# Optimization experiments

Measured on AMD Instinct MI355X. Metric: run time of the kernel, lower is better.

## Reference

```python
import jax, jax.numpy as jnp
import numpy as np

HEADS = 32
K_TOP = 512  # top-k tokens gathered from KV


def conv3d(x, w, b=None, pad=0, groups=1):
    # x: [B,C,D,H,W], w: [O, I/groups, kd,kh,kw]
    out = jax.lax.conv_general_dilated(
        x, w, window_strides=(1, 1, 1), padding=[(pad, pad)] * 3,
        dimension_numbers=("NCDHW", "OIDHW", "NCDHW"), feature_group_count=groups)
    if b is not None:
        out = out + b[None, :, None, None, None]
    return out


def setup_inputs() -> dict:
    key = jax.random.key(0)
    ks = jax.random.split(key, 10)
    B, C, D, H, W = 2, 256, 16, 16, 16
    p = lambda i, shape: (jax.random.normal(ks[i], shape, jnp.float32) * 0.02)
    return {
        "x_kv": jax.random.normal(ks[0], (B, C, D, H, W), jnp.float32),
        "x_q": jax.random.normal(ks[1], (B, C, D, H, W), jnp.float32),
        "w_spa": p(2, (1, 2, 7, 7, 7)),            # SpatialAttention conv, no bias
        "w_kv": p(3, (C, 2 * C)), "b_kv": jnp.zeros((2 * C,), jnp.float32),
        "w_q": p(4, (C, C)), "b_q": jnp.zeros((C,), jnp.float32),
        "w_proj": p(5, (C, C)), "b_proj": jnp.zeros((C,), jnp.float32),
        "w_dw": p(6, (C, 1, 3, 3, 3)), "b_dw": jnp.zeros((C,), jnp.float32),  # depthwise 3x3x3
        "w_pw": p(7, (C, C, 1, 1, 1)), "b_pw": jnp.zeros((C,), jnp.float32),  # pointwise 1x1x1
    }


def reference(x_kv, x_q, w_spa, w_kv, b_kv, w_q, b_q, w_proj, b_proj,
              w_dw, b_dw, w_pw, b_pw):
    B, C, D, H, W = x_kv.shape
    N = D * H * W
    hd = C // HEADS
    scale = hd ** -0.5

    # SpatialAttention: channel mean/max -> conv(2->1, k=7, pad=3) -> sigmoid
    avg = jnp.mean(x_kv, axis=1, keepdims=True)
    mx = jnp.max(x_kv, axis=1, keepdims=True)
    spa = jax.nn.sigmoid(conv3d(jnp.concatenate([avg, mx], axis=1), w_spa, None, pad=3))
    scores = spa.reshape(B, N)                      # [B, N]
    _, idx = jax.lax.top_k(scores, K_TOP)           # [B, K] (descending, like torch.topk)

    # Full K/V projection over all N tokens (as in original), then gather top-k
    xkv_t = x_kv.reshape(B, C, N).transpose(0, 2, 1)        # [B, N, C]
    kv = xkv_t @ w_kv + b_kv                                 # [B, N, 2C]
    k_full, v_full = kv[..., :C], kv[..., C:]
    k_g = jnp.take_along_axis(k_full, idx[:, :, None], axis=1)  # [B, K, C]
    v_g = jnp.take_along_axis(v_full, idx[:, :, None], axis=1)
    k_g = k_g.reshape(B, K_TOP, HEADS, hd).transpose(0, 2, 1, 3)  # [B, h, K, d]
    v_g = v_g.reshape(B, K_TOP, HEADS, hd).transpose(0, 2, 1, 3)

    # Queries over all Nq tokens
    xq_t = x_q.reshape(B, C, N).transpose(0, 2, 1)           # [B, N, C]
    q = (xq_t @ w_q + b_q).reshape(B, N, HEADS, hd).transpose(0, 2, 1, 3)  # [B, h, N, d]

    attn = jax.nn.softmax(jnp.einsum('bhnd,bhkd->bhnk', q, k_g) * scale, axis=-1)
    out = jnp.einsum('bhnk,bhkd->bhnd', attn, v_g)           # [B, h, N, d]
    out = out.transpose(0, 2, 1, 3).reshape(B, N, C)
    out = out @ w_proj + b_proj
    out = out.transpose(0, 2, 1).reshape(B, C, D, H, W)

    # DWconv residual on full (ungathered) V
    v_vol = v_full.transpose(0, 2, 1).reshape(B, C, D, H, W)
    res = conv3d(conv3d(v_vol, w_dw, b_dw, pad=1, groups=C), w_pw, b_pw)
    return out + res
```

## Files before the change

### kernel.cpp

```cpp
#include <hip/hip_runtime.h>
#include <hip/hip_bf16.h>

typedef short bf16x8 __attribute__((ext_vector_type(8)));
typedef float f32x4 __attribute__((ext_vector_type(4)));

constexpr int CN = 256, NV = 4096, KTOP = 512;

static __device__ __forceinline__ unsigned short f2bf(float f) {
  __hip_bfloat16 h = __float2bfloat16(f);
  return *(unsigned short*)&h;
}
static __device__ __forceinline__ unsigned pack2(float a, float b) {
  return (unsigned)f2bf(a) | ((unsigned)f2bf(b) << 16);
}
static __device__ __forceinline__ float bf2f(unsigned short u) {
  return __uint_as_float(((unsigned)u) << 16);
}
static __device__ __forceinline__ unsigned packtrunc(float a, float b) {
  return (__float_as_uint(a) >> 16) | (__float_as_uint(b) & 0xFFFF0000u);
}

__global__ void __launch_bounds__(256) k_tcast2(const float* __restrict__ srcA,
                                                const float* __restrict__ srcB,
                                                unsigned short* __restrict__ dstA,
                                                unsigned short* __restrict__ dstB) {
  __shared__ float tile[64 * 65];
  int z = blockIdx.z, b = z & 1;
  const float* s = (z < 2 ? srcA : srcB) + (size_t)b * CN * NV;
  unsigned short* d = (z < 2 ? dstA : dstB) + (size_t)b * NV * 256;
  int c0 = blockIdx.y * 64, n0 = blockIdx.x * 64;
  int t = threadIdx.x;
  for (int i = 0; i < 16; ++i) {
    int id = i * 256 + t, c = id >> 6, n = id & 63;
    tile[c * 65 + n] = s[(size_t)(c0 + c) * NV + n0 + n];
  }
  __syncthreads();
  int n = t & 63, part = t >> 6;
  unsigned w[8];
#pragma unroll
  for (int k = 0; k < 8; ++k)
    w[k] = pack2(tile[(part * 16 + 2 * k) * 65 + n], tile[(part * 16 + 2 * k + 1) * 65 + n]);
  uint4* p = (uint4*)&d[(size_t)(n0 + n) * 256 + c0 + part * 16];
  p[0] = make_uint4(w[0], w[1], w[2], w[3]);
  p[1] = make_uint4(w[4], w[5], w[6], w[7]);
}

__global__ void __launch_bounds__(256) k_wprep(const float* __restrict__ wkv,
                                               const float* __restrict__ wq,
                                               const float* __restrict__ wproj,
                                               const float* __restrict__ wpw,
                                               unsigned short* __restrict__ wv_t,
                                               unsigned short* __restrict__ wq_t,
                                               unsigned short* __restrict__ wcat,
                                               unsigned short* __restrict__ wk_t) {
  __shared__ float tile[64 * 65];
  int role = blockIdx.z;
  int j0 = blockIdx.x * 64, c0 = blockIdx.y * 64;
  int t = threadIdx.x;
  if (role == 3) {
    int j = t >> 2, part = t & 3;
    const float* s = &wpw[(size_t)(j0 + j) * 256 + c0 + part * 16];
    unsigned w[8];
#pragma unroll
    for (int k = 0; k < 8; ++k) w[k] = pack2(s[2 * k], s[2 * k + 1]);
    uint4* p = (uint4*)&wcat[(size_t)(j0 + j) * 512 + 256 + c0 + part * 16];
    p[0] = make_uint4(w[0], w[1], w[2], w[3]);
    p[1] = make_uint4(w[4], w[5], w[6], w[7]);
    return;
  }
  const float* src; int srcLD, srcOff; unsigned short* dst; int dstLD;
  if (role == 0)      { src = wkv;   srcLD = 512; srcOff = 256; dst = wv_t; dstLD = 256; }
  else if (role == 1) { src = wq;    srcLD = 256; srcOff = 0;   dst = wq_t; dstLD = 256; }
  else if (role == 4) { src = wkv;   srcLD = 512; srcOff = 0;   dst = wk_t; dstLD = 256; }
  else                { src = wproj; srcLD = 256; srcOff = 0;   dst = wcat; dstLD = 512; }
  for (int i = 0; i < 16; ++i) {
    int id = i * 256 + t, c = id >> 6, j = id & 63;
    tile[c * 65 + j] = src[(size_t)(c0 + c) * srcLD + srcOff + j0 + j];
  }
  __syncthreads();
  int j = t & 63, part = t >> 6;
  unsigned w[8];
#pragma unroll
  for (int k = 0; k < 8; ++k)
    w[k] = pack2(tile[(part * 16 + 2 * k) * 65 + j], tile[(part * 16 + 2 * k + 1) * 65 + j]);
  uint4* p = (uint4*)&dst[(size_t)(j0 + j) * dstLD + c0 + part * 16];
  p[0] = make_uint4(w[0], w[1], w[2], w[3]);
  p[1] = make_uint4(w[4], w[5], w[6], w[7]);
}

__global__ void __launch_bounds__(256) k_reduce(const float* __restrict__ xkv,
                                                float* __restrict__ avgmx) {
  __shared__ float ssum[256], smax[256];
  int blk = blockIdx.x;
  int b = blk >> 7, n0 = (blk & 127) * 32;
  int t = threadIdx.x, cg = t >> 5, nl = t & 31;
  int n = n0 + nl;
  const float* p = xkv + (size_t)b * CN * NV + (size_t)cg * 32 * NV + n;
  float s = 0.f, m = -1e30f;
  for (int i = 0; i < 32; ++i) {
    float v = p[(size_t)i * NV];
    s += v; m = fmaxf(m, v);
  }
  ssum[t] = s; smax[t] = m;
  __syncthreads();
  if (cg == 0) {
    for (int g = 1; g < 8; ++g) { s += ssum[g * 32 + nl]; m = fmaxf(m, smax[g * 32 + nl]); }
    avgmx[(b * 2 + 0) * NV + n] = s * (1.0f / 256.0f);
    avgmx[(b * 2 + 1) * NV + n] = m;
  }
}

__global__ void __launch_bounds__(256) k_spa(const float* __restrict__ avgmx,
                                             const float* __restrict__ wspa,
                                             float* __restrict__ scores) {
  __shared__ float vol[2 * 4096];
  __shared__ float ws[686];
  int b = blockIdx.x >> 5, chunk = blockIdx.x & 31;
  int tid = threadIdx.x;
  for (int t = tid; t < 8192; t += 256) vol[t] = avgmx[b * 8192 + t];
  for (int t = tid; t < 686; t += 256) ws[t] = wspa[t];
  __syncthreads();
  int ci = tid & 1;
  int n = chunk * 128 + (tid >> 1);
  int d = n >> 8, h = (n >> 4) & 15, w = n & 15;
  const float* vb = vol + ci * 4096;
  const float* wb = ws + ci * 343;
  float acc = 0.f;
  for (int kd = 0; kd < 7; ++kd) {
    int zd = d - 3 + kd; if ((unsigned)zd >= 16u) continue;
    for (int kh = 0; kh < 7; ++kh) {
      int zh = h - 3 + kh; if ((unsigned)zh >= 16u) continue;
      const float* row = vb + zd * 256 + zh * 16;
      const float* wr = wb + kd * 49 + kh * 7;
#pragma unroll
      for (int kw = 0; kw < 7; ++kw) {
        int zw = w - 3 + kw;
        if ((unsigned)zw < 16u) acc += row[zw] * wr[kw];
      }
    }
  }
  acc += __shfl_xor(acc, 1);
  if (ci == 0) scores[b * NV + n] = 1.0f / (1.0f + expf(-acc));
}

__global__ void __launch_bounds__(1024) k_topk(const float* __restrict__ scores,
                                               int* __restrict__ idx) {
  __shared__ unsigned sv[4096];
  __shared__ int sB;
  __shared__ unsigned sSub, scnt;
  __shared__ unsigned hist[256];
  __shared__ int wsum[16];
  int b = blockIdx.x, tid = threadIdx.x;
  for (int t = tid; t < 4096; t += 1024) sv[t] = __float_as_uint(scores[b * NV + t]);
  if (tid == 0) scnt = 0;
  unsigned prefix = 0;
  int r = 512;
  for (int shift = 24; shift >= 0; shift -= 8) {
    if (tid < 256) hist[tid] = 0;
    __syncthreads();
    unsigned maskhi = (shift == 24) ? 0u : (0xFFFFFFFFu << (shift + 8));
    for (int i = 0; i < 4; ++i) {
      unsigned v = sv[tid + i * 1024];
      if ((v & maskhi) == prefix) atomicAdd(&hist[(v >> shift) & 255], 1u);
    }
    __syncthreads();
    if (tid < 64) {
      int lane = tid;
      unsigned h0 = hist[lane * 4 + 0], h1 = hist[lane * 4 + 1];
      unsigned h2 = hist[lane * 4 + 2], h3 = hist[lane * 4 + 3];
      unsigned s = h0 + h1 + h2 + h3;
      for (int off = 1; off < 64; off <<= 1) {
        unsigned y = __shfl_down(s, off);
        if (lane + off < 64) s += y;
      }
      unsigned tail = __shfl_down(s, 1);
      if (lane == 63) tail = 0;
      unsigned s3 = tail + h3, s2 = s3 + h2, s1 = s2 + h1, s0 = s1 + h0;
      unsigned sx[5] = {s0, s1, s2, s3, tail};
#pragma unroll
      for (int i = 0; i < 4; ++i)
        if (sx[i] >= (unsigned)r && sx[i + 1] < (unsigned)r) { sB = lane * 4 + i; sSub = sx[i + 1]; }
    }
    __syncthreads();
    prefix |= ((unsigned)sB) << shift;
    r -= (int)sSub;
    __syncthreads();
  }
  unsigned vstar = prefix;
  for (int i = 0; i < 4; ++i) {
    int t = tid * 4 + i;
    if (sv[t] > vstar) { unsigned p = atomicAdd(&scnt, 1u); idx[b * KTOP + p] = t; }
  }
  __syncthreads();
  int base = (int)scnt;
  int loc = 0;
  for (int i = 0; i < 4; ++i) loc += (sv[tid * 4 + i] == vstar);
  int lane = tid & 63, w = tid >> 6;
  int x = loc;
  for (int off = 1; off < 64; off <<= 1) {
    int y = __shfl_up(x, off);
    if (lane >= off) x += y;
  }
  if (lane == 63) wsum[w] = x;
  __syncthreads();
  int wbase = 0;
  for (int i = 0; i < w; ++i) wbase += wsum[i];
  int excl = wbase + x - loc;
  for (int i = 0; i < 4; ++i) {
    int t = tid * 4 + i;
    if (sv[t] == vstar) {
      if (excl < r) idx[b * KTOP + base + excl] = t;
      ++excl;
    }
  }
}

__global__ void __launch_bounds__(256) k_qv(const unsigned short* __restrict__ xkv_t,
                                            const unsigned short* __restrict__ xq_t,
                                            const unsigned short* __restrict__ wv_t,
                                            const unsigned short* __restrict__ wq_t,
                                            const float* __restrict__ bkv,
                                            const float* __restrict__ bq,
                                            unsigned short* __restrict__ v_nc,
                                            unsigned short* __restrict__ qh) {
  __shared__ unsigned short Als[128 * 40];
  __shared__ unsigned short Bls[128 * 40];
  int role = blockIdx.z;
  int b = role & 1;
  bool isQ = role >= 2;
  const unsigned short* A = isQ ? wq_t : wv_t;
  const unsigned short* B = (isQ ? xq_t : xkv_t) + (size_t)b * NV * 256;
  const float* bias = isQ ? bq : (bkv + 256);
  int n0 = blockIdx.x * 128, j0 = blockIdx.y * 128;
  int t = threadIdx.x;
  int wave = t >> 6, lane = t & 63;
  int l15 = lane & 15, q = lane >> 4, q8 = q * 8;
  int wj = (wave >> 1) * 64, wn = (wave & 1) * 64;
  f32x4 acc[4][4] = {};
  int ar = t >> 1, ah = t & 1;
  for (int c0 = 0; c0 < 256; c0 += 32) {
    __syncthreads();
    {
      const unsigned short* sa = &A[(size_t)(j0 + ar) * 256 + c0 + ah * 16];
      *(uint4*)&Als[ar * 40 + ah * 16]     = *(const uint4*)&sa[0];
      *(uint4*)&Als[ar * 40 + ah * 16 + 8] = *(const uint4*)&sa[8];
      const unsigned short* sb = &B[(size_t)(n0 + ar) * 256 + c0 + ah * 16];
      *(uint4*)&Bls[ar * 40 + ah * 16]     = *(const uint4*)&sb[0];
      *(uint4*)&Bls[ar * 40 + ah * 16 + 8] = *(const uint4*)&sb[8];
    }
    __syncthreads();
    bf16x8 af[4], bf[4];
#pragma unroll
    for (int mt = 0; mt < 4; ++mt)
      af[mt] = *(const bf16x8*)&Als[(wj + mt * 16 + l15) * 40 + q8];
#pragma unroll
    for (int nt = 0; nt < 4; ++nt)
      bf[nt] = *(const bf16x8*)&Bls[(wn + nt * 16 + l15) * 40 + q8];
#pragma unroll
    for (int mt = 0; mt < 4; ++mt)
#pragma unroll
      for (int nt = 0; nt < 4; ++nt)
        acc[mt][nt] = __builtin_amdgcn_mfma_f32_16x16x32_bf16(af[mt], bf[nt], acc[mt][nt], 0, 0, 0);
  }
#pragma unroll
  for (int mt = 0; mt < 4; ++mt) {
    int jb = j0 + wj + mt * 16 + q * 4;
    float4 b4 = *(const float4*)&bias[jb];
#pragma unroll
    for (int nt = 0; nt < 4; ++nt) {
      int n = n0 + wn + nt * 16 + l15;
      float v0 = acc[mt][nt][0] + b4.x;
      float v1 = acc[mt][nt][1] + b4.y;
      float v2 = acc[mt][nt][2] + b4.z;
      float v3 = acc[mt][nt][3] + b4.w;
      uint2 pk = make_uint2(pack2(v0, v1), pack2(v2, v3));
      if (isQ) {
        int h = jb >> 3, d0 = jb & 7;
        *(uint2*)&qh[((size_t)(b * 32 + h) * NV + n) * 8 + d0] = pk;
      } else {
        *(uint2*)&v_nc[((size_t)b * NV + n) * 256 + jb] = pk;
      }
    }
  }
}

__global__ void __launch_bounds__(256) k_kg(const unsigned short* __restrict__ xkv_t,
                                            const unsigned short* __restrict__ wk_t,
                                            const float* __restrict__ bkv,
                                            const int* __restrict__ map,
                                            unsigned short* __restrict__ kg) {
  __shared__ unsigned short Als[128 * 40];
  __shared__ unsigned short Bls[128 * 40];
  const float kscale = 0.35355339059327373f * 1.4426950408889634f;
  int b = blockIdx.z;
  int m0 = blockIdx.x * 128, j0 = blockIdx.y * 128;
  int t = threadIdx.x;
  int wave = t >> 6, lane = t & 63;
  int l15 = lane & 15, q = lane >> 4, q8 = q * 8;
  int wj = (wave >> 1) * 64, wn = (wave & 1) * 64;
  int ar = t >> 1, ah = t & 1;
  int nrow = map[b * KTOP + m0 + ar];
  const unsigned short* Bbase = xkv_t + (size_t)b * NV * 256;
  f32x4 acc[4][4] = {};
  for (int c0 = 0; c0 < 256; c0 += 32) {
    __syncthreads();
    {
      const unsigned short* sa = &wk_t[(size_t)(j0 + ar) * 256 + c0 + ah * 16];
      *(uint4*)&Als[ar * 40 + ah * 16]     = *(const uint4*)&sa[0];
      *(uint4*)&Als[ar * 40 + ah * 16 + 8] = *(const uint4*)&sa[8];
      const unsigned short* sb = &Bbase[(size_t)nrow * 256 + c0 + ah * 16];
      *(uint4*)&Bls[ar * 40 + ah * 16]     = *(const uint4*)&sb[0];
      *(uint4*)&Bls[ar * 40 + ah * 16 + 8] = *(const uint4*)&sb[8];
    }
    __syncthreads();
    bf16x8 af[4], bfr[4];
#pragma unroll
    for (int mt = 0; mt < 4; ++mt)
      af[mt] = *(const bf16x8*)&Als[(wj + mt * 16 + l15) * 40 + q8];
#pragma unroll
    for (int nt = 0; nt < 4; ++nt)
      bfr[nt] = *(const bf16x8*)&Bls[(wn + nt * 16 + l15) * 40 + q8];
#pragma unroll
    for (int mt = 0; mt < 4; ++mt)
#pragma unroll
      for (int nt = 0; nt < 4; ++nt)
        acc[mt][nt] = __builtin_amdgcn_mfma_f32_16x16x32_bf16(af[mt], bfr[nt], acc[mt][nt], 0, 0, 0);
  }
#pragma unroll
  for (int mt = 0; mt < 4; ++mt) {
    int jb = j0 + wj + mt * 16 + q * 4;
    int h = jb >> 3, d0 = jb & 7;
    float4 b4 = *(const float4*)&bkv[jb];
#pragma unroll
    for (int nt = 0; nt < 4; ++nt) {
      int m = m0 + wn + nt * 16 + l15;
      float v0 = (acc[mt][nt][0] + b4.x) * kscale;
      float v1 = (acc[mt][nt][1] + b4.y) * kscale;
      float v2 = (acc[mt][nt][2] + b4.z) * kscale;
      float v3 = (acc[mt][nt][3] + b4.w) * kscale;
      uint2 pk = make_uint2(pack2(v0, v1), pack2(v2, v3));
      *(uint2*)&kg[((size_t)(b * 32 + h) * KTOP + m) * 8 + d0] = pk;
    }
  }
}

__global__ void __launch_bounds__(256) k_vt(const unsigned short* __restrict__ v_nc,
                                            const int* __restrict__ idx,
                                            unsigned short* __restrict__ vt) {
  int bh = blockIdx.x;
  int b = bh >> 5, h = bh & 31;
  int t = threadIdx.x;
  unsigned short* dst = vt + (size_t)bh * 16 * 512;
  for (int i = t; i < 512; i += 256) dst[8 * 512 + i] = 0x3F80;
  for (int i = t; i < 512 * 7; i += 256) dst[9 * 512 + i] = 0;
  const int* ib = idx + b * KTOP;
  for (int kk = t; kk < 512; kk += 256) {
    uint4 v = *(const uint4*)&v_nc[((size_t)b * NV + ib[kk]) * 256 + h * 8];
    unsigned short tmp[8];
    *(uint4*)tmp = v;
    int kc = kk >> 5, ka = kk & 31;
    int s = (ka < 16) ? ((ka >> 2) * 8 + (ka & 3))
                      : (((ka - 16) >> 2) * 8 + (ka & 3) + 4);
    int col = kc * 32 + s;
#pragma unroll
    for (int d = 0; d < 8; ++d) dst[d * 512 + col] = tmp[d];
  }
}

__global__ void __launch_bounds__(256) k_fattn(const unsigned short* __restrict__ qh,
                                               const unsigned short* __restrict__ kg,
                                               const unsigned short* __restrict__ vt,
                                               unsigned short* __restrict__ aoydw) {
  int bh = blockIdx.x;
  int b = bh >> 5, h = bh & 31;
  int t = threadIdx.x, wave = t >> 6, lane = t & 63;
  int l15 = lane & 15, quad = lane >> 4;
  int n0 = blockIdx.y * 128 + wave * 32;
  bf16x8 q0 = {}, q1 = {};
  if (quad == 0) {
    q0 = *(const bf16x8*)&qh[((size_t)bh * NV + n0 + l15) * 8];
    q1 = *(const bf16x8*)&qh[((size_t)bh * NV + n0 + 16 + l15) * 8];
  }
  const unsigned short* kbase = kg + (size_t)bh * KTOP * 8;
  const unsigned short* vbase = vt + (size_t)bh * 16 * 512;
  f32x4 acc0 = {0.f, 0.f, 0.f, 0.f}, acc1 = {0.f, 0.f, 0.f, 0.f};
  bf16x8 kA0 = {}, kA1 = {};
  if (quad == 0) {
    kA0 = *(const bf16x8*)&kbase[(size_t)l15 * 8];
    kA1 = *(const bf16x8*)&kbase[(size_t)(16 + l15) * 8];
  }
  for (int kc = 0; kc < 16; ++kc) {
    bf16x8 nA0 = {}, nA1 = {};
    if (quad == 0 && kc < 15) {
      nA0 = *(const bf16x8*)&kbase[(size_t)(kc * 32 + 32 + l15) * 8];
      nA1 = *(const bf16x8*)&kbase[(size_t)(kc * 32 + 48 + l15) * 8];
    }
    bf16x8 bV = *(const bf16x8*)&vbase[(size_t)l15 * 512 + kc * 32 + quad * 8];
    f32x4 z = {0.f, 0.f, 0.f, 0.f};
    f32x4 s00 = __builtin_amdgcn_mfma_f32_16x16x32_bf16(kA0, q0, z, 0, 0, 0);
    f32x4 s01 = __builtin_amdgcn_mfma_f32_16x16x32_bf16(kA1, q0, z, 0, 0, 0);
    f32x4 s10 = __builtin_amdgcn_mfma_f32_16x16x32_bf16(kA0, q1, z, 0, 0, 0);
    f32x4 s11 = __builtin_amdgcn_mfma_f32_16x16x32_bf16(kA1, q1, z, 0, 0, 0);
    uint4 P0, P1;
    P0.x = packtrunc(__builtin_amdgcn_exp2f(s00[0]), __builtin_amdgcn_exp2f(s00[1]));
    P0.y = packtrunc(__builtin_amdgcn_exp2f(s00[2]), __builtin_amdgcn_exp2f(s00[3]));
    P0.z = packtrunc(__builtin_amdgcn_exp2f(s01[0]), __builtin_amdgcn_exp2f(s01[1]));
    P0.w = packtrunc(__builtin_amdgcn_exp2f(s01[2]), __builtin_amdgcn_exp2f(s01[3]));
    P1.x = packtrunc(__builtin_amdgcn_exp2f(s10[0]), __builtin_amdgcn_exp2f(s10[1]));
    P1.y = packtrunc(__builtin_amdgcn_exp2f(s10[2]), __builtin_amdgcn_exp2f(s10[3]));
    P1.z = packtrunc(__builtin_amdgcn_exp2f(s11[0]), __builtin_amdgcn_exp2f(s11[1]));
    P1.w = packtrunc(__builtin_amdgcn_exp2f(s11[2]), __builtin_amdgcn_exp2f(s11[3]));
    acc0 = __builtin_amdgcn_mfma_f32_16x16x32_bf16(*(bf16x8*)&P0, bV, acc0, 0, 0, 0);
    acc1 = __builtin_amdgcn_mfma_f32_16x16x32_bf16(*(bf16x8*)&P1, bV, acc1, 0, 0, 0);
    kA0 = nA0; kA1 = nA1;
  }
#pragma unroll
  for (int tq = 0; tq < 2; ++tq) {
    f32x4 a = tq ? acc1 : acc0;
#pragma unroll
    for (int r = 0; r < 4; ++r) {
      float se = __shfl(a[r], quad * 16 + 8);
      float o = a[r] * (1.0f / se);
      if (l15 < 8) {
        int n = n0 + tq * 16 + quad * 4 + r;
        aoydw[((size_t)b * NV + n) * 512 + h * 8 + l15] = f2bf(o);
      }
    }
  }
}

__global__ void __launch_bounds__(256) k_dw(const unsigned short* __restrict__ v_nc,
                                            const float* __restrict__ wdw,
                                            const float* __restrict__ bdw,
                                            unsigned short* __restrict__ aoydw) {
  int c = threadIdx.x;
  int b = blockIdx.y;
  float wr[27];
#pragma unroll
  for (int i = 0; i < 27; ++i) wr[i] = wdw[c * 27 + i];
  float bias = bdw[c];
  const unsigned short* src = v_nc + (size_t)b * NV * 256 + c;
  unsigned short* dst = aoydw + (size_t)b * NV * 512 + 256 + c;
  int n = blockIdx.x * 4;
  int d = n >> 8, h = (n >> 4) & 15, w = n & 15;
  float a0 = bias, a1 = bias, a2 = bias, a3 = bias;
#pragma unroll
  for (int kd = 0; kd < 3; ++kd) {
    int zd = d - 1 + kd; bool okd = (unsigned)zd < 16u;
#pragma unroll
    for (int kh = 0; kh < 3; ++kh) {
      int zh = h - 1 + kh; bool okh = okd && ((unsigned)zh < 16u);
      int rowb = zd * 256 + zh * 16;
      float v[6];
#pragma unroll
      for (int i = 0; i < 6; ++i) {
        int zw = w - 1 + i;
        bool ok = okh && ((unsigned)zw < 16u);
        v[i] = ok ? bf2f(src[(size_t)(rowb + zw) * 256]) : 0.f;
      }
      const float* wp = &wr[kd * 9 + kh * 3];
      a0 = fmaf(v[0], wp[0], fmaf(v[1], wp[1], fmaf(v[2], wp[2], a0)));
      a1 = fmaf(v[1], wp[0], fmaf(v[2], wp[1], fmaf(v[3], wp[2], a1)));
      a2 = fmaf(v[2], wp[0], fmaf(v[3], wp[1], fmaf(v[4], wp[2], a2)));
      a3 = fmaf(v[3], wp[0], fmaf(v[4], wp[1], fmaf(v[5], wp[2], a3)));
    }
  }
  dst[(size_t)(n + 0) * 512] = f2bf(a0);
  dst[(size_t)(n + 1) * 512] = f2bf(a1);
  dst[(size_t)(n + 2) * 512] = f2bf(a2);
  dst[(size_t)(n + 3) * 512] = f2bf(a3);
}

__global__ void __launch_bounds__(256) k_final(const unsigned short* __restrict__ aoydw,
                                               const unsigned short* __restrict__ wcat,
                                               const float* __restrict__ bproj,
                                               const float* __restrict__ bpw,
                                               float* __restrict__ out) {
  __shared__ unsigned short Als[64 * 40];
  __shared__ unsigned short Bls[128 * 40];
  int n0 = blockIdx.x * 64, j0 = blockIdx.y * 128, b = blockIdx.z;
  int t = threadIdx.x;
  int wave = t >> 6, lane = t & 63;
  int l15 = lane & 15, q = lane >> 4, q8 = q * 8;
  int wn = (wave >> 1) * 32, wjj = (wave & 1) * 64;
  f32x4 acc[2][4] = {};
  const unsigned short* Abase = aoydw + (size_t)b * NV * 512;
  int ar = t >> 2, aq = t & 3;
  int br = t >> 1, bhh = t & 1;
  for (int c0 = 0; c0 < 512; c0 += 32) {
    __syncthreads();
    *(uint4*)&Als[ar * 40 + aq * 8] =
        *(const uint4*)&Abase[(size_t)(n0 + ar) * 512 + c0 + aq * 8];
    const unsigned short* sb = &wcat[(size_t)(j0 + br) * 512 + c0 + bhh * 16];
    *(uint4*)&Bls[br * 40 + bhh * 16]     = *(const uint4*)&sb[0];
    *(uint4*)&Bls[br * 40 + bhh * 16 + 8] = *(const uint4*)&sb[8];
    __syncthreads();
    bf16x8 af[2], bf[4];
#pragma unroll
    for (int mt = 0; mt < 2; ++mt)
      af[mt] = *(const bf16x8*)&Als[(wn + mt * 16 + l15) * 40 + q8];
#pragma unroll
    for (int nt = 0; nt < 4; ++nt)
      bf[nt] = *(const bf16x8*)&Bls[(wjj + nt * 16 + l15) * 40 + q8];
#pragma unroll
    for (int mt = 0; mt < 2; ++mt)
#pragma unroll
      for (int nt = 0; nt < 4; ++nt)
        acc[mt][nt] = __builtin_amdgcn_mfma_f32_16x16x32_bf16(af[mt], bf[nt], acc[mt][nt], 0, 0, 0);
  }
#pragma unroll
  for (int nt = 0; nt < 4; ++nt) {
    int j = j0 + wjj + nt * 16 + l15;
    float bl = bproj[j] + bpw[j];
#pragma unroll
    for (int mt = 0; mt < 2; ++mt) {
      int n = n0 + wn + mt * 16 + q * 4;
      float4 r = make_float4(acc[mt][nt][0] + bl, acc[mt][nt][1] + bl,
                             acc[mt][nt][2] + bl, acc[mt][nt][3] + bl);
      *(float4*)&out[(size_t)(b * 256 + j) * NV + n] = r;
    }
  }
}

extern "C" void kernel_launch(void* const* d_in, const int* in_sizes, int n_in,
                              void* d_out, int out_size, void* d_ws, size_t ws_size,
                              hipStream_t stream) {
  const float* x_kv   = (const float*)d_in[0];
  const float* x_q    = (const float*)d_in[1];
  const float* w_spa  = (const float*)d_in[2];
  const float* w_kv   = (const float*)d_in[3];
  const float* b_kv   = (const float*)d_in[4];
  const float* w_q    = (const float*)d_in[5];
  const float* b_q    = (const float*)d_in[6];
  const float* w_proj = (const float*)d_in[7];
  const float* b_proj = (const float*)d_in[8];
  const float* w_dw   = (const float*)d_in[9];
  const float* b_dw   = (const float*)d_in[10];
  const float* w_pw   = (const float*)d_in[11];
  const float* b_pw   = (const float*)d_in[12];
  float* out = (float*)d_out;

  const size_t MB = 1024 * 1024;
  char* ws = (char*)d_ws;
  unsigned short* xkv_t = (unsigned short*)(ws);
  unsigned short* xq_t  = (unsigned short*)(ws + 4 * MB);
  unsigned short* v_nc  = (unsigned short*)(ws + 8 * MB);
  unsigned short* qh    = (unsigned short*)(ws + 12 * MB);
  unsigned short* aoydw = (unsigned short*)(ws + 16 * MB);
  unsigned short* kg    = (unsigned short*)(ws + 24 * MB);
  unsigned short* vt    = (unsigned short*)(ws + 24 * MB + 512 * 1024);
  unsigned short* wv_t  = (unsigned short*)(ws + 26 * MB);
  unsigned short* wq_t  = (unsigned short*)(ws + 26 * MB + 131072);
  unsigned short* wcat  = (unsigned short*)(ws + 26 * MB + 262144);
  unsigned short* wk_t  = (unsigned short*)(ws + 26 * MB + 524288);
  float*          avgmx = (float*)(ws + 27 * MB);
  float*          scores= (float*)(ws + 27 * MB + 65536);
  int*            idx   = (int*)  (ws + 27 * MB + 98304);

  k_tcast2<<<dim3(64, 4, 4), 256, 0, stream>>>(x_kv, x_q, xkv_t, xq_t);
  k_wprep<<<dim3(4, 4, 5), 256, 0, stream>>>(w_kv, w_q, w_proj, w_pw, wv_t, wq_t, wcat, wk_t);
  k_reduce<<<256, 256, 0, stream>>>(x_kv, avgmx);
  k_spa<<<64, 256, 0, stream>>>(avgmx, w_spa, scores);
  k_topk<<<2, 1024, 0, stream>>>(scores, idx);
  k_qv<<<dim3(32, 2, 4), 256, 0, stream>>>(xkv_t, xq_t, wv_t, wq_t, b_kv, b_q, v_nc, qh);
  k_kg<<<dim3(4, 2, 2), 256, 0, stream>>>(xkv_t, wk_t, b_kv, idx, kg);
  k_vt<<<64, 256, 0, stream>>>(v_nc, idx, vt);
  k_fattn<<<dim3(64, 32), 256, 0, stream>>>(qh, kg, vt, aoydw);
  k_dw<<<dim3(1024, 2), 256, 0, stream>>>(v_nc, w_dw, b_dw, aoydw);
  k_final<<<dim3(64, 2, 2), 256, 0, stream>>>(aoydw, wcat, b_proj, b_pw, out);
}
```

Measured before the change: 215.3 us.

## Merge reduce into transpose-cast launch and fuse K-gather GEMM with V transpose

The channel mean/max reduction now runs as an extra z-slice of the transpose-cast kernel, which removes one launch. The K-gather projection and the V gather/transpose are merged into one kernel. The K GEMM is also retiled from 16 large LDS-staged blocks to 128 blocks in which each wave computes one 16x16 tile straight from global memory. This cuts launch count and spreads the small GEMM over more CUs, at the cost of redundant global loads that no longer go through LDS.

Result: faster. 205.2 us (-4.7%).

```diff
diff --git a/kernel.cpp b/kernel.cpp
--- a/kernel.cpp
+++ b/kernel.cpp
@@ -23,13 +23,36 @@
 __global__ void __launch_bounds__(256) k_tcast2(const float* __restrict__ srcA,
                                                 const float* __restrict__ srcB,
                                                 unsigned short* __restrict__ dstA,
-                                                unsigned short* __restrict__ dstB) {
+                                                unsigned short* __restrict__ dstB,
+                                                float* __restrict__ avgmx) {
   __shared__ float tile[64 * 65];
-  int z = blockIdx.z, b = z & 1;
+  int z = blockIdx.z;
+  int t = threadIdx.x;
+  if (z == 4) {
+    __shared__ float ssum[256], smax[256];
+    int blk = blockIdx.y * 64 + blockIdx.x;
+    int b = blk >> 7, n0 = (blk & 127) * 32;
+    int cg = t >> 5, nl = t & 31;
+    int n = n0 + nl;
+    const float* p = srcA + (size_t)b * CN * NV + (size_t)cg * 32 * NV + n;
+    float s = 0.f, m = -1e30f;
+    for (int i = 0; i < 32; ++i) {
+      float v = p[(size_t)i * NV];
+      s += v; m = fmaxf(m, v);
+    }
+    ssum[t] = s; smax[t] = m;
+    __syncthreads();
+    if (cg == 0) {
+      for (int g = 1; g < 8; ++g) { s += ssum[g * 32 + nl]; m = fmaxf(m, smax[g * 32 + nl]); }
+      avgmx[(b * 2 + 0) * NV + n] = s * (1.0f / 256.0f);
+      avgmx[(b * 2 + 1) * NV + n] = m;
+    }
+    return;
+  }
+  int b = z & 1;
   const float* s = (z < 2 ? srcA : srcB) + (size_t)b * CN * NV;
   unsigned short* d = (z < 2 ? dstA : dstB) + (size_t)b * NV * 256;
   int c0 = blockIdx.y * 64, n0 = blockIdx.x * 64;
-  int t = threadIdx.x;
   for (int i = 0; i < 16; ++i) {
     int id = i * 256 + t, c = id >> 6, n = id & 63;
     tile[c * 65 + n] = s[(size_t)(c0 + c) * NV + n0 + n];
@@ -86,28 +109,6 @@
   uint4* p = (uint4*)&dst[(size_t)(j0 + j) * dstLD + c0 + part * 16];
   p[0] = make_uint4(w[0], w[1], w[2], w[3]);
   p[1] = make_uint4(w[4], w[5], w[6], w[7]);
-}
-
-__global__ void __launch_bounds__(256) k_reduce(const float* __restrict__ xkv,
-                                                float* __restrict__ avgmx) {
-  __shared__ float ssum[256], smax[256];
-  int blk = blockIdx.x;
-  int b = blk >> 7, n0 = (blk & 127) * 32;
-  int t = threadIdx.x, cg = t >> 5, nl = t & 31;
-  int n = n0 + nl;
-  const float* p = xkv + (size_t)b * CN * NV + (size_t)cg * 32 * NV + n;
-  float s = 0.f, m = -1e30f;
-  for (int i = 0; i < 32; ++i) {
-    float v = p[(size_t)i * NV];
-    s += v; m = fmaxf(m, v);
-  }
-  ssum[t] = s; smax[t] = m;
-  __syncthreads();
-  if (cg == 0) {
-    for (int g = 1; g < 8; ++g) { s += ssum[g * 32 + nl]; m = fmaxf(m, smax[g * 32 + nl]); }
-    avgmx[(b * 2 + 0) * NV + n] = s * (1.0f / 256.0f);
-    avgmx[(b * 2 + 1) * NV + n] = m;
-  }
 }
 
 __global__ void __launch_bounds__(256) k_spa(const float* __restrict__ avgmx,
@@ -284,87 +285,62 @@
   }
 }
 
-__global__ void __launch_bounds__(256) k_kg(const unsigned short* __restrict__ xkv_t,
-                                            const unsigned short* __restrict__ wk_t,
-                                            const float* __restrict__ bkv,
-                                            const int* __restrict__ map,
-                                            unsigned short* __restrict__ kg) {
-  __shared__ unsigned short Als[128 * 40];
-  __shared__ unsigned short Bls[128 * 40];
+__global__ void __launch_bounds__(256) k_kgvt(const unsigned short* __restrict__ xkv_t,
+                                              const unsigned short* __restrict__ wk_t,
+                                              const float* __restrict__ bkv,
+                                              const int* __restrict__ map,
+                                              const unsigned short* __restrict__ v_nc,
+                                              unsigned short* __restrict__ kg,
+                                              unsigned short* __restrict__ vt) {
+  int b = blockIdx.z;
+  int bx = blockIdx.x;
+  int t = threadIdx.x;
+  if (bx >= 128) {
+    int h = bx - 128;
+    int bh = b * 32 + h;
+    unsigned short* dst = vt + (size_t)bh * 16 * 512;
+    for (int i = t; i < 512; i += 256) dst[8 * 512 + i] = 0x3F80;
+    for (int i = t; i < 512 * 7; i += 256) dst[9 * 512 + i] = 0;
+    const int* ib = map + b * KTOP;
+    for (int kk = t; kk < 512; kk += 256) {
+      uint4 v = *(const uint4*)&v_nc[((size_t)b * NV + ib[kk]) * 256 + h * 8];
+      unsigned short tmp[8];
+      *(uint4*)tmp = v;
+      int kc = kk >> 5, ka = kk & 31;
+      int s = (ka < 16) ? ((ka >> 2) * 8 + (ka & 3))
+                        : (((ka - 16) >> 2) * 8 + (ka & 3) + 4);
+      int col = kc * 32 + s;
+#pragma unroll
+      for (int d = 0; d < 8; ++d) dst[d * 512 + col] = tmp[d];
+    }
+    return;
+  }
   const float kscale = 0.35355339059327373f * 1.4426950408889634f;
-  int b = blockIdx.z;
-  int m0 = blockIdx.x * 128, j0 = blockIdx.y * 128;
-  int t = threadIdx.x;
   int wave = t >> 6, lane = t & 63;
-  int l15 = lane & 15, q = lane >> 4, q8 = q * 8;
-  int wj = (wave >> 1) * 64, wn = (wave & 1) * 64;
-  int ar = t >> 1, ah = t & 1;
-  int nrow = map[b * KTOP + m0 + ar];
-  const unsigned short* Bbase = xkv_t + (size_t)b * NV * 256;
-  f32x4 acc[4][4] = {};
-  for (int c0 = 0; c0 < 256; c0 += 32) {
-    __syncthreads();
-    {
-      const unsigned short* sa = &wk_t[(size_t)(j0 + ar) * 256 + c0 + ah * 16];
-      *(uint4*)&Als[ar * 40 + ah * 16]     = *(const uint4*)&sa[0];
-      *(uint4*)&Als[ar * 40 + ah * 16 + 8] = *(const uint4*)&sa[8];
-      const unsigned short* sb = &Bbase[(size_t)nrow * 256 + c0 + ah * 16];
-      *(uint4*)&Bls[ar * 40 + ah * 16]     = *(const uint4*)&sb[0];
-      *(uint4*)&Bls[ar * 40 + ah * 16 + 8] = *(const uint4*)&sb[8];
-    }
-    __syncthreads();
-    bf16x8 af[4], bfr[4];
-#pragma unroll
-    for (int mt = 0; mt < 4; ++mt)
-      af[mt] = *(const bf16x8*)&Als[(wj + mt * 16 + l15) * 40 + q8];
-#pragma unroll
-    for (int nt = 0; nt < 4; ++nt)
-      bfr[nt] = *(const bf16x8*)&Bls[(wn + nt * 16 + l15) * 40 + q8];
-#pragma unroll
-    for (int mt = 0; mt < 4; ++mt)
-#pragma unroll
-      for (int nt = 0; nt < 4; ++nt)
-        acc[mt][nt] = __builtin_amdgcn_mfma_f32_16x16x32_bf16(af[mt], bfr[nt], acc[mt][nt], 0, 0, 0);
-  }
-#pragma unroll
-  for (int mt = 0; mt < 4; ++mt) {
-    int jb = j0 + wj + mt * 16 + q * 4;
-    int h = jb >> 3, d0 = jb & 7;
-    float4 b4 = *(const float4*)&bkv[jb];
-#pragma unroll
-    for (int nt = 0; nt < 4; ++nt) {
-      int m = m0 + wn + nt * 16 + l15;
-      float v0 = (acc[mt][nt][0] + b4.x) * kscale;
-      float v1 = (acc[mt][nt][1] + b4.y) * kscale;
-      float v2 = (acc[mt][nt][2] + b4.z) * kscale;
-      float v3 = (acc[mt][nt][3] + b4.w) * kscale;
-      uint2 pk = make_uint2(pack2(v0, v1), pack2(v2, v3));
-      *(uint2*)&kg[((size_t)(b * 32 + h) * KTOP + m) * 8 + d0] = pk;
-    }
-  }
-}
-
-__global__ void __launch_bounds__(256) k_vt(const unsigned short* __restrict__ v_nc,
-                                            const int* __restrict__ idx,
-                                            unsigned short* __restrict__ vt) {
-  int bh = blockIdx.x;
-  int b = bh >> 5, h = bh & 31;
-  int t = threadIdx.x;
-  unsigned short* dst = vt + (size_t)bh * 16 * 512;
-  for (int i = t; i < 512; i += 256) dst[8 * 512 + i] = 0x3F80;
-  for (int i = t; i < 512 * 7; i += 256) dst[9 * 512 + i] = 0;
-  const int* ib = idx + b * KTOP;
-  for (int kk = t; kk < 512; kk += 256) {
-    uint4 v = *(const uint4*)&v_nc[((size_t)b * NV + ib[kk]) * 256 + h * 8];
-    unsigned short tmp[8];
-    *(uint4*)tmp = v;
-    int kc = kk >> 5, ka = kk & 31;
-    int s = (ka < 16) ? ((ka >> 2) * 8 + (ka & 3))
-                      : (((ka - 16) >> 2) * 8 + (ka & 3) + 4);
-    int col = kc * 32 + s;
-#pragma unroll
-    for (int d = 0; d < 8; ++d) dst[d * 512 + col] = tmp[d];
-  }
+  int l15 = lane & 15, quad = lane >> 4;
+  int tile_id = bx * 4 + wave;
+  int kt = tile_id & 31, jt = tile_id >> 5;
+  int m0 = kt * 16, j0 = jt * 16;
+  int nrow = map[b * KTOP + m0 + l15];
+  const unsigned short* Arow = wk_t + (size_t)(j0 + l15) * 256 + quad * 8;
+  const unsigned short* Brow = xkv_t + (size_t)b * NV * 256 + (size_t)nrow * 256 + quad * 8;
+  f32x4 acc = {0.f, 0.f, 0.f, 0.f};
+#pragma unroll
+  for (int s = 0; s < 8; ++s) {
+    bf16x8 af = *(const bf16x8*)&Arow[s * 32];
+    bf16x8 bf = *(const bf16x8*)&Brow[s * 32];
+    acc = __builtin_amdgcn_mfma_f32_16x16x32_bf16(af, bf, acc, 0, 0, 0);
+  }
+  int h = (j0 >> 3) + (quad >> 1), d0b = (quad & 1) * 4;
+  int jb = j0 + quad * 4;
+  float4 b4 = *(const float4*)&bkv[jb];
+  int m = m0 + l15;
+  float v0 = (acc[0] + b4.x) * kscale;
+  float v1 = (acc[1] + b4.y) * kscale;
+  float v2 = (acc[2] + b4.z) * kscale;
+  float v3 = (acc[3] + b4.w) * kscale;
+  *(uint2*)&kg[((size_t)(b * 32 + h) * KTOP + m) * 8 + d0b] =
+      make_uint2(pack2(v0, v1), pack2(v2, v3));
 }
 
 __global__ void __launch_bounds__(256) k_fattn(const unsigned short* __restrict__ qh,
@@ -557,14 +533,12 @@
   float*          scores= (float*)(ws + 27 * MB + 65536);
   int*            idx   = (int*)  (ws + 27 * MB + 98304);
 
-  k_tcast2<<<dim3(64, 4, 4), 256, 0, stream>>>(x_kv, x_q, xkv_t, xq_t);
+  k_tcast2<<<dim3(64, 4, 5), 256, 0, stream>>>(x_kv, x_q, xkv_t, xq_t, avgmx);
   k_wprep<<<dim3(4, 4, 5), 256, 0, stream>>>(w_kv, w_q, w_proj, w_pw, wv_t, wq_t, wcat, wk_t);
-  k_reduce<<<256, 256, 0, stream>>>(x_kv, avgmx);
   k_spa<<<64, 256, 0, stream>>>(avgmx, w_spa, scores);
   k_topk<<<2, 1024, 0, stream>>>(scores, idx);
   k_qv<<<dim3(32, 2, 4), 256, 0, stream>>>(xkv_t, xq_t, wv_t, wq_t, b_kv, b_q, v_nc, qh);
-  k_kg<<<dim3(4, 2, 2), 256, 0, stream>>>(xkv_t, wk_t, b_kv, idx, kg);
-  k_vt<<<64, 256, 0, stream>>>(v_nc, idx, vt);
+  k_kgvt<<<dim3(160, 1, 2), 256, 0, stream>>>(xkv_t, wk_t, b_kv, idx, v_nc, kg, vt);
   k_fattn<<<dim3(64, 32), 256, 0, stream>>>(qh, kg, vt, aoydw);
   k_dw<<<dim3(1024, 2), 256, 0, stream>>>(v_nc, w_dw, b_dw, aoydw);
   k_final<<<dim3(64, 2, 2), 256, 0, stream>>>(aoydw, wcat, b_proj, b_pw, out);
```
